# Optimization experiments

Hardware: AMD Instinct MI355X
Metric: run time of the kernel (lower is better)

Reference implementation:

```python
import jax, jax.numpy as jnp
import numpy as np

NH = 8      # num_heads
NP_ = 4     # num_points

def setup_inputs() -> dict:
    key = jax.random.key(0)
    ks = jax.random.split(key, 12)
    B, N, C = 8, 4096, 256
    query = jax.random.normal(ks[0], (B, N, C), jnp.float32)
    value = jax.random.normal(ks[1], (B, N, C), jnp.float32)
    reference_points = jax.random.uniform(ks[2], (B, N, 2), jnp.float32)
    xav = lambda k, i, o: jax.random.normal(k, (i, o), jnp.float32) * np.sqrt(2.0 / (i + o)).astype(np.float32)
    W_off = jax.random.normal(ks[3], (C, NH * NP_ * 2), jnp.float32) * 0.02  # small offsets (orig inits to 0)
    b_off = jax.random.normal(ks[4], (NH * NP_ * 2,), jnp.float32) * 0.02
    W_attn = xav(ks[5], C, NH * NP_)
    b_attn = jnp.zeros((NH * NP_,), jnp.float32)
    W_val = xav(ks[6], C, C)
    b_val = jnp.zeros((C,), jnp.float32)
    W_out = xav(ks[7], C, C)
    b_out = jnp.zeros((C,), jnp.float32)
    return dict(query=query, value=value, reference_points=reference_points,
                W_off=W_off, b_off=b_off, W_attn=W_attn, b_attn=b_attn,
                W_val=W_val, b_val=b_val, W_out=W_out, b_out=b_out)

def _deform_attn(query, value, reference_points, W_off, b_off, W_attn, b_attn, W_val, b_val, W_out, b_out):
    B, N, C = query.shape
    HW = value.shape[1]
    H = W = int(np.sqrt(HW))  # static
    hd = C // NH
    # value projection -> [B, NH, H*W, hd]
    vals = (value @ W_val + b_val).reshape(B, H, W, NH, hd)
    vals = vals.transpose(0, 3, 1, 2, 4).reshape(B, NH, H * W, hd)
    # offsets [B,N,NH,P,2] in [-0.5,0.5]; attention weights softmax over P
    off = jnp.tanh((query @ W_off + b_off).reshape(B, N, NH, NP_, 2)) * 0.5
    attn = jax.nn.softmax((query @ W_attn + b_attn).reshape(B, N, NH, NP_), axis=-1)
    # sampling locations in [0,1], then grid coords in [-1,1] (x=width, y=height)
    loc = jnp.clip(reference_points[:, :, None, None, :] + off, 0.0, 1.0)
    g = loc * 2.0 - 1.0
    # torch grid_sample, align_corners=False: pixel = (g+1)*size/2 - 0.5
    x = (g[..., 0] + 1.0) * (W * 0.5) - 0.5
    y = (g[..., 1] + 1.0) * (H * 0.5) - 0.5
    x0f = jnp.floor(x); y0f = jnp.floor(y)
    wx1 = x - x0f; wx0 = 1.0 - wx1
    wy1 = y - y0f; wy0 = 1.0 - wy1
    x0 = x0f.astype(jnp.int32); x1 = x0 + 1
    y0 = y0f.astype(jnp.int32); y1 = y0 + 1

    def corner(xi, yi, w):  # xi,yi,w: [B,N,NH,P]; zero padding outside
        valid = (xi >= 0) & (xi < W) & (yi >= 0) & (yi < H)
        idx = jnp.clip(yi, 0, H - 1) * W + jnp.clip(xi, 0, W - 1)
        idx_h = idx.transpose(0, 2, 1, 3).reshape(B, NH, N * NP_)      # [B,NH,N*P]
        gat = jnp.take_along_axis(vals, idx_h[..., None], axis=2)      # [B,NH,N*P,hd]
        wv = jnp.where(valid, w, 0.0).transpose(0, 2, 1, 3).reshape(B, NH, N * NP_)
        return gat * wv[..., None]

    sampled = (corner(x0, y0, wx0 * wy0) + corner(x1, y0, wx1 * wy0)
               + corner(x0, y1, wx0 * wy1) + corner(x1, y1, wx1 * wy1))
    sampled = sampled.reshape(B, NH, N, NP_, hd)
    attn_h = attn.transpose(0, 2, 1, 3)                                 # [B,NH,N,P]
    out = jnp.einsum('bhnpd,bhnp->bnhd', sampled, attn_h).reshape(B, N, C)
    return out @ W_out + b_out  # dropout is identity in eval

def reference(query, value, reference_points, W_off, b_off, W_attn, b_attn, W_val, b_val, W_out, b_out):
    return _deform_attn(query, value, reference_points, W_off, b_off, W_attn, b_attn, W_val, b_val, W_out, b_out)
```

## Files before the change

### kernel.cpp

```cpp
#include <hip/hip_runtime.h>
#include <math.h>

#define NHEAD 8
#define NPT 4
#define HDIM 32
#define IMG 64
#define CDIM 256
#define NQ 4096
#define BATCH 8
#define MTOT (BATCH * NQ)

typedef __attribute__((ext_vector_type(8))) short bf16x8;
typedef __attribute__((ext_vector_type(4))) float f32x4;

__device__ __forceinline__ unsigned short f2b(float f) {
    union { float f; unsigned u; } v; v.f = f;
    unsigned r = (v.u + 0x7FFFu + ((v.u >> 16) & 1u)) >> 16;
    return (unsigned short)r;
}
__device__ __forceinline__ float b2f(unsigned short u) {
    union { unsigned u; float f; } v; v.u = ((unsigned)u) << 16;
    return v.f;
}

#define SWZ(row, col) ((col) ^ (((row) & 7) << 3))

__device__ __forceinline__ void gload16(const void* src, void* ldsbase) {
    __builtin_amdgcn_global_load_lds(
        (const __attribute__((address_space(1))) void*)src,
        (__attribute__((address_space(3))) void*)ldsbase, 16, 0, 0);
}


__global__ __launch_bounds__(256)
void cvt_weights_kernel(const float* __restrict__ Wv, const float* __restrict__ Wo,
                        const float* __restrict__ Woff, const float* __restrict__ Wattn,
                        const float* __restrict__ boff, const float* __restrict__ battn,
                        unsigned short* __restrict__ Wv_t, unsigned short* __restrict__ Wo_t,
                        unsigned short* __restrict__ Wl_h, unsigned short* __restrict__ Wl_l,
                        float* __restrict__ bias_lin)
{
    int tid = blockIdx.x * 256 + threadIdx.x;
    int n = tid & 255, k = tid >> 8;
    Wv_t[n * 256 + k] = f2b(Wv[k * 256 + n]);
    Wo_t[n * 256 + k] = f2b(Wo[k * 256 + n]);
    if (tid < 128 * 256) {
        int nn = tid >> 8;
        int kk = tid & 255;
        float v = (nn < 64) ? Woff[kk * 64 + nn]
                : (nn < 96) ? Wattn[kk * 32 + (nn - 64)] : 0.f;
        unsigned short hi = f2b(v);
        unsigned short lo = f2b(v - b2f(hi));
        Wl_h[nn * 256 + kk] = hi;
        Wl_l[nn * 256 + kk] = lo;
    }
    if (tid < 128)
        bias_lin[tid] = (tid < 64) ? boff[tid] : (tid < 96) ? battn[tid - 64] : 0.f;
}

__global__ __launch_bounds__(256)
void lin_gemm_kernel(const float* __restrict__ Q,
                     const unsigned short* __restrict__ Wl_h,
                     const unsigned short* __restrict__ Wl_l,
                     const float* __restrict__ bias,
                     float* __restrict__ lin)
{
    __shared__ unsigned short Ah[128][64], Al[128][64];
    __shared__ unsigned short Bh[128][64], Bl[128][64];

    const int tid  = threadIdx.x;
    const int lane = tid & 63;
    const int wid  = tid >> 6;
    const int gm = ((blockIdx.x & 7) << 12) + ((blockIdx.x >> 3) << 7);
    const int wr = (wid >> 1) * 64;
    const int wc = (wid & 1) * 64;
    const int l15 = lane & 15;
    const int lk  = (lane >> 4) * 8;
    const int rl  = lane >> 3;
    const int ch  = (lane & 7) ^ (rl & 7);

    f32x4 acc[4][4];
    #pragma unroll
    for (int m = 0; m < 4; ++m)
        #pragma unroll
        for (int n = 0; n < 4; ++n)
            #pragma unroll
            for (int r = 0; r < 4; ++r) acc[m][n][r] = 0.f;

    for (int k0 = 0; k0 < 256; k0 += 64) {
        #pragma unroll
        for (int it = 0; it < 4; ++it) {
            const int br = it * 32 + wid * 8;
            gload16(&Wl_h[(size_t)(br + rl) * 256 + k0 + ch * 8], &Bh[br][0]);
            gload16(&Wl_l[(size_t)(br + rl) * 256 + k0 + ch * 8], &Bl[br][0]);
        }
        #pragma unroll
        for (int it = 0; it < 4; ++it) {
            const int chunk = it * 256 + tid;
            const int row = chunk >> 3;
            const int kc  = (chunk & 7) << 3;
            const float4* src = (const float4*)&Q[(size_t)(gm + row) * 256 + k0 + kc];
            const float4 a = src[0], b = src[1];
            float f[8] = {a.x, a.y, a.z, a.w, b.x, b.y, b.z, b.w};
            unsigned short h[8], l[8];
            #pragma unroll
            for (int j = 0; j < 8; ++j) {
                h[j] = f2b(f[j]);
                l[j] = f2b(f[j] - b2f(h[j]));
            }
            const int sc = SWZ(row, kc);
            *(uint4*)&Ah[row][sc] = *(const uint4*)h;
            *(uint4*)&Al[row][sc] = *(const uint4*)l;
        }
        __syncthreads();

        #pragma unroll
        for (int kk = 0; kk < 64; kk += 32) {
            bf16x8 ah[4], al[4];
            #pragma unroll
            for (int m = 0; m < 4; ++m) {
                const int r = wr + m * 16 + l15;
                const int c = SWZ(r, kk + lk);
                ah[m] = *(const bf16x8*)&Ah[r][c];
                al[m] = *(const bf16x8*)&Al[r][c];
            }
            if (wc == 0) {
                bf16x8 bh[4], bl[4];
                #pragma unroll
                for (int n = 0; n < 4; ++n) {
                    const int r = n * 16 + l15;
                    const int c = SWZ(r, kk + lk);
                    bh[n] = *(const bf16x8*)&Bh[r][c];
                    bl[n] = *(const bf16x8*)&Bl[r][c];
                }
                #pragma unroll
                for (int m = 0; m < 4; ++m)
                    #pragma unroll
                    for (int n = 0; n < 4; ++n) {
                        acc[m][n] = __builtin_amdgcn_mfma_f32_16x16x32_bf16(ah[m], bh[n], acc[m][n], 0, 0, 0);
                        acc[m][n] = __builtin_amdgcn_mfma_f32_16x16x32_bf16(ah[m], bl[n], acc[m][n], 0, 0, 0);
                        acc[m][n] = __builtin_amdgcn_mfma_f32_16x16x32_bf16(al[m], bh[n], acc[m][n], 0, 0, 0);
                    }
            } else {
                bf16x8 bh[2], bl[2];
                #pragma unroll
                for (int n = 0; n < 2; ++n) {
                    const int r = 64 + n * 16 + l15;
                    const int c = SWZ(r, kk + lk);
                    bh[n] = *(const bf16x8*)&Bh[r][c];
                    bl[n] = *(const bf16x8*)&Bl[r][c];
                }
                #pragma unroll
                for (int m = 0; m < 4; ++m)
                    #pragma unroll
                    for (int n = 0; n < 2; ++n) {
                        acc[m][n] = __builtin_amdgcn_mfma_f32_16x16x32_bf16(ah[m], bh[n], acc[m][n], 0, 0, 0);
                        acc[m][n] = __builtin_amdgcn_mfma_f32_16x16x32_bf16(ah[m], bl[n], acc[m][n], 0, 0, 0);
                        acc[m][n] = __builtin_amdgcn_mfma_f32_16x16x32_bf16(al[m], bh[n], acc[m][n], 0, 0, 0);
                    }
            }
        }
        __syncthreads();
    }

    const int cr = (lane >> 4) * 4;
    #pragma unroll
    for (int n = 0; n < 4; ++n) {
        const int col = wc + n * 16 + l15;
        if (col < 96) {
            const float bv = bias[col];
            #pragma unroll
            for (int m = 0; m < 4; ++m)
                #pragma unroll
                for (int r = 0; r < 4; ++r) {
                    const int row = gm + wr + m * 16 + cr + r;
                    lin[(size_t)row * 96 + col] = acc[m][n][r] + bv;
                }
        }
    }
}

template<bool A_F32, bool OUT_BF16>
__global__ __launch_bounds__(256)
void gemm_bf16_kernel(const void* __restrict__ Ap,
                      const unsigned short* __restrict__ Bt,
                      const float* __restrict__ bias,
                      void* __restrict__ C)
{
    __shared__ unsigned short As[128][64];
    __shared__ unsigned short Bs[128][64];

    const int tid  = threadIdx.x;
    const int lane = tid & 63;
    const int wid  = tid >> 6;
    const int gm = ((blockIdx.x & 7) << 12) + ((blockIdx.x >> 3) << 7);
    const int gn = blockIdx.y * 128;
    const int wr = (wid >> 1) * 64;
    const int wc = (wid & 1) * 64;
    const int l15 = lane & 15;
    const int lk  = (lane >> 4) * 8;
    const int rl  = lane >> 3;
    const int ch  = (lane & 7) ^ (rl & 7);

    f32x4 acc[4][4];
    #pragma unroll
    for (int m = 0; m < 4; ++m)
        #pragma unroll
        for (int n = 0; n < 4; ++n)
            #pragma unroll
            for (int r = 0; r < 4; ++r) acc[m][n][r] = 0.f;

    for (int k0 = 0; k0 < 256; k0 += 64) {
        #pragma unroll
        for (int it = 0; it < 4; ++it) {
            const int br = it * 32 + wid * 8;
            gload16(&Bt[(size_t)(gn + br + rl) * 256 + k0 + ch * 8], &Bs[br][0]);
        }
        if (A_F32) {
            #pragma unroll
            for (int it = 0; it < 4; ++it) {
                const int chunk = it * 256 + tid;
                const int row = chunk >> 3;
                const int kc  = (chunk & 7) << 3;
                const float4* src = (const float4*)&((const float*)Ap)[(size_t)(gm + row) * 256 + k0 + kc];
                const float4 a = src[0], b = src[1];
                float f[8] = {a.x, a.y, a.z, a.w, b.x, b.y, b.z, b.w};
                unsigned short h[8];
                #pragma unroll
                for (int j = 0; j < 8; ++j) h[j] = f2b(f[j]);
                *(uint4*)&As[row][SWZ(row, kc)] = *(const uint4*)h;
            }
        } else {
            #pragma unroll
            for (int it = 0; it < 4; ++it) {
                const int br = it * 32 + wid * 8;
                gload16(&((const unsigned short*)Ap)[(size_t)(gm + br + rl) * 256 + k0 + ch * 8], &As[br][0]);
            }
        }
        __syncthreads();

        #pragma unroll
        for (int kk = 0; kk < 64; kk += 32) {
            bf16x8 a[4], b[4];
            #pragma unroll
            for (int m = 0; m < 4; ++m) {
                const int r = wr + m * 16 + l15;
                a[m] = *(const bf16x8*)&As[r][SWZ(r, kk + lk)];
            }
            #pragma unroll
            for (int n = 0; n < 4; ++n) {
                const int r = wc + n * 16 + l15;
                b[n] = *(const bf16x8*)&Bs[r][SWZ(r, kk + lk)];
            }
            #pragma unroll
            for (int m = 0; m < 4; ++m)
                #pragma unroll
                for (int n = 0; n < 4; ++n)
                    acc[m][n] = __builtin_amdgcn_mfma_f32_16x16x32_bf16(a[m], b[n], acc[m][n], 0, 0, 0);
        }
        __syncthreads();
    }

    const int cr = (lane >> 4) * 4;
    #pragma unroll
    for (int n = 0; n < 4; ++n) {
        const int col = gn + wc + n * 16 + l15;
        const float bv = bias[col];
        #pragma unroll
        for (int m = 0; m < 4; ++m) {
            #pragma unroll
            for (int r = 0; r < 4; ++r) {
                const int row = gm + wr + m * 16 + cr + r;
                const float v = acc[m][n][r] + bv;
                if (OUT_BF16)
                    ((unsigned short*)C)[(size_t)row * 256 + col] = f2b(v);
                else
                    ((float*)C)[(size_t)row * 256 + col] = v;
            }
        }
    }
}

__global__ __launch_bounds__(256)
void sample_gather_kernel(const unsigned short* __restrict__ projv,
                          const float* __restrict__ lin,
                          const float* __restrict__ refp,
                          unsigned short* __restrict__ sampled)
{
    __shared__ float4 s_w[8][32];
    __shared__ unsigned s_xy[8][32];

    const int i = blockIdx.x;
    const int b = i & 7;
    const int bn0 = (b << 12) + ((i >> 3) << 3);
    const int t = threadIdx.x;

    {
        const int sub = t >> 5;
        const int q = t & 31;
        const int h = q >> 2;
        const int p = q & 3;
        const int bn = bn0 + sub;
        const float2 rp = *(const float2*)&refp[(size_t)bn * 2];
        const float2 ol = *(const float2*)&lin[(size_t)bn * 96 + h * 8 + p * 2];
        const float al  = lin[(size_t)bn * 96 + 64 + q];

        float mx = al;
        mx = fmaxf(mx, __shfl_xor(mx, 1));
        mx = fmaxf(mx, __shfl_xor(mx, 2));
        float e = expf(al - mx);
        float s = e;
        s += __shfl_xor(s, 1);
        s += __shfl_xor(s, 2);
        const float aw = e / s;

        const float lx = fminf(fmaxf(rp.x + tanhf(ol.x) * 0.5f, 0.f), 1.f);
        const float ly = fminf(fmaxf(rp.y + tanhf(ol.y) * 0.5f, 0.f), 1.f);
        const float x = lx * (float)IMG - 0.5f;
        const float y = ly * (float)IMG - 0.5f;
        const float x0f = floorf(x), y0f = floorf(y);
        const int x0 = (int)x0f, y0 = (int)y0f;
        const float wx1 = x - x0f, wx0 = 1.f - wx1;
        const float wy1 = y - y0f, wy0 = 1.f - wy1;
        const bool vx0 = (x0 >= 0), vx1 = (x0 + 1 < IMG);
        const bool vy0 = (y0 >= 0), vy1 = (y0 + 1 < IMG);
        float4 w;
        w.x = (vx0 && vy0) ? wx0 * wy0 * aw : 0.f;
        w.y = (vx1 && vy0) ? wx1 * wy0 * aw : 0.f;
        w.z = (vx0 && vy1) ? wx0 * wy1 * aw : 0.f;
        w.w = (vx1 && vy1) ? wx1 * wy1 * aw : 0.f;
        const int x0c = min(max(x0, 0), IMG - 1), x1c = min(max(x0 + 1, 0), IMG - 1);
        const int y0c = min(max(y0, 0), IMG - 1), y1c = min(max(y0 + 1, 0), IMG - 1);
        s_w[sub][q] = w;
        s_xy[sub][q] = (unsigned)x0c | ((unsigned)x1c << 8) | ((unsigned)y0c << 16) | ((unsigned)y1c << 24);
    }
    __syncthreads();

    const int l = t & 63;
    const int h2 = l >> 3;
    const int cp = l & 7;
    const unsigned short* vbase = projv + ((size_t)b << 20) + h2 * HDIM + cp * 4;

    #pragma unroll
    for (int pass = 0; pass < 2; ++pass) {
        const int sub = (t >> 6) + pass * 4;
        const int bn = bn0 + sub;

        float a0 = 0.f, a1 = 0.f, a2 = 0.f, a3 = 0.f;
        #pragma unroll
        for (int p = 0; p < 4; ++p) {
            const float4 w = s_w[sub][h2 * 4 + p];
            const unsigned xy = s_xy[sub][h2 * 4 + p];
            const int x0 = xy & 255, x1 = (xy >> 8) & 255;
            const int y0 = (xy >> 16) & 255, y1 = xy >> 24;
            const uint2 u00 = *(const uint2*)&vbase[(((y0 << 6) + x0) << 8)];
            const uint2 u01 = *(const uint2*)&vbase[(((y0 << 6) + x1) << 8)];
            const uint2 u10 = *(const uint2*)&vbase[(((y1 << 6) + x0) << 8)];
            const uint2 u11 = *(const uint2*)&vbase[(((y1 << 6) + x1) << 8)];
            a0 += w.x * b2f((unsigned short)(u00.x & 0xffff)) + w.y * b2f((unsigned short)(u01.x & 0xffff))
                + w.z * b2f((unsigned short)(u10.x & 0xffff)) + w.w * b2f((unsigned short)(u11.x & 0xffff));
            a1 += w.x * b2f((unsigned short)(u00.x >> 16)) + w.y * b2f((unsigned short)(u01.x >> 16))
                + w.z * b2f((unsigned short)(u10.x >> 16)) + w.w * b2f((unsigned short)(u11.x >> 16));
            a2 += w.x * b2f((unsigned short)(u00.y & 0xffff)) + w.y * b2f((unsigned short)(u01.y & 0xffff))
                + w.z * b2f((unsigned short)(u10.y & 0xffff)) + w.w * b2f((unsigned short)(u11.y & 0xffff));
            a3 += w.x * b2f((unsigned short)(u00.y >> 16)) + w.y * b2f((unsigned short)(u01.y >> 16))
                + w.z * b2f((unsigned short)(u10.y >> 16)) + w.w * b2f((unsigned short)(u11.y >> 16));
        }
        uint2 outp;
        outp.x = (unsigned)f2b(a0) | ((unsigned)f2b(a1) << 16);
        outp.y = (unsigned)f2b(a2) | ((unsigned)f2b(a3) << 16);
        *(uint2*)&sampled[(size_t)bn * 256 + h2 * HDIM + cp * 4] = outp;
    }
}

extern "C" void kernel_launch(void* const* d_in, const int* in_sizes, int n_in,
                              void* d_out, int out_size, void* d_ws, size_t ws_size,
                              hipStream_t stream)
{
    const float* query  = (const float*)d_in[0];
    const float* value  = (const float*)d_in[1];
    const float* refp   = (const float*)d_in[2];
    const float* W_off  = (const float*)d_in[3];
    const float* b_off  = (const float*)d_in[4];
    const float* W_attn = (const float*)d_in[5];
    const float* b_attn = (const float*)d_in[6];
    const float* W_val  = (const float*)d_in[7];
    const float* b_val  = (const float*)d_in[8];
    const float* W_out  = (const float*)d_in[9];
    const float* b_out  = (const float*)d_in[10];
    float* out = (float*)d_out;

    char* ws = (char*)d_ws;
    unsigned short* projv    = (unsigned short*)ws; ws += (size_t)MTOT * 256 * 2;
    unsigned short* sampled  = (unsigned short*)ws; ws += (size_t)MTOT * 256 * 2;
    float*          lin      = (float*)ws;          ws += (size_t)MTOT * 96 * 4;
    unsigned short* Wv_t     = (unsigned short*)ws; ws += 256 * 256 * 2;
    unsigned short* Wo_t     = (unsigned short*)ws; ws += 256 * 256 * 2;
    unsigned short* Wl_h     = (unsigned short*)ws; ws += 128 * 256 * 2;
    unsigned short* Wl_l     = (unsigned short*)ws; ws += 128 * 256 * 2;
    float*          bias_lin = (float*)ws;          ws += 128 * 4;

    dim3 blk(256);

    cvt_weights_kernel<<<dim3(256), blk, 0, stream>>>(W_val, W_out, W_off, W_attn, b_off, b_attn,
                                                      Wv_t, Wo_t, Wl_h, Wl_l, bias_lin);

    gemm_bf16_kernel<true, true><<<dim3(MTOT / 128, 2), blk, 0, stream>>>(value, Wv_t, b_val, projv);

    lin_gemm_kernel<<<dim3(MTOT / 128), blk, 0, stream>>>(query, Wl_h, Wl_l, bias_lin, lin);

    sample_gather_kernel<<<dim3(MTOT / 8), blk, 0, stream>>>(projv, lin, refp, sampled);

    gemm_bf16_kernel<false, false><<<dim3(MTOT / 128, 2), blk, 0, stream>>>(sampled, Wo_t, b_out, out);
}
```

Before: 73.93 us.

## Merge value-projection and offset/attention GEMMs into one launch with smaller LDS

Combines the value projection GEMM and the offset/attention linear GEMM into a single kernel launch of 768 blocks. The first 512 blocks compute projv and the remaining 256 compute lin. The lin path now uses a K-step of 32 with a matching 4-row swizzle, so LDS per block drops from 64KB to 32KB. The aim is to remove a launch boundary, let the two independent GEMMs overlap across CUs, and raise occupancy. The cost is twice as many k-iterations and barriers in the lin blocks, plus an uneven block workload mix.

```diff
diff --git a/kernel.cpp b/kernel.cpp
--- a/kernel.cpp
+++ b/kernel.cpp
@@ -23,7 +23,8 @@
     return v.f;
 }
 
-#define SWZ(row, col) ((col) ^ (((row) & 7) << 3))
+#define SWZ(row, col)   ((col) ^ (((row) & 7) << 3))
+#define SWZ32(row, col) ((col) ^ (((row) & 3) << 3))
 
 __device__ __forceinline__ void gload16(const void* src, void* ldsbase) {
     __builtin_amdgcn_global_load_lds(
@@ -59,25 +60,25 @@
 }
 
 __global__ __launch_bounds__(256)
-void lin_gemm_kernel(const float* __restrict__ Q,
-                     const unsigned short* __restrict__ Wl_h,
-                     const unsigned short* __restrict__ Wl_l,
-                     const float* __restrict__ bias,
-                     float* __restrict__ lin)
+void fused_gemms_kernel(const float* __restrict__ value,
+                        const float* __restrict__ query,
+                        const unsigned short* __restrict__ Wv_t,
+                        const unsigned short* __restrict__ Wl_h,
+                        const unsigned short* __restrict__ Wl_l,
+                        const float* __restrict__ b_val,
+                        const float* __restrict__ bias_lin,
+                        unsigned short* __restrict__ projv,
+                        float* __restrict__ lin)
 {
-    __shared__ unsigned short Ah[128][64], Al[128][64];
-    __shared__ unsigned short Bh[128][64], Bl[128][64];
+    __shared__ char smem[32768];
 
     const int tid  = threadIdx.x;
     const int lane = tid & 63;
     const int wid  = tid >> 6;
-    const int gm = ((blockIdx.x & 7) << 12) + ((blockIdx.x >> 3) << 7);
     const int wr = (wid >> 1) * 64;
     const int wc = (wid & 1) * 64;
     const int l15 = lane & 15;
     const int lk  = (lane >> 4) * 8;
-    const int rl  = lane >> 3;
-    const int ch  = (lane & 7) ^ (rl & 7);
 
     f32x4 acc[4][4];
     #pragma unroll
@@ -87,40 +88,114 @@
             #pragma unroll
             for (int r = 0; r < 4; ++r) acc[m][n][r] = 0.f;
 
-    for (int k0 = 0; k0 < 256; k0 += 64) {
-        #pragma unroll
-        for (int it = 0; it < 4; ++it) {
-            const int br = it * 32 + wid * 8;
-            gload16(&Wl_h[(size_t)(br + rl) * 256 + k0 + ch * 8], &Bh[br][0]);
-            gload16(&Wl_l[(size_t)(br + rl) * 256 + k0 + ch * 8], &Bl[br][0]);
-        }
-        #pragma unroll
-        for (int it = 0; it < 4; ++it) {
-            const int chunk = it * 256 + tid;
-            const int row = chunk >> 3;
-            const int kc  = (chunk & 7) << 3;
-            const float4* src = (const float4*)&Q[(size_t)(gm + row) * 256 + k0 + kc];
-            const float4 a = src[0], b = src[1];
-            float f[8] = {a.x, a.y, a.z, a.w, b.x, b.y, b.z, b.w};
-            unsigned short h[8], l[8];
-            #pragma unroll
-            for (int j = 0; j < 8; ++j) {
-                h[j] = f2b(f[j]);
-                l[j] = f2b(f[j] - b2f(h[j]));
-            }
-            const int sc = SWZ(row, kc);
-            *(uint4*)&Ah[row][sc] = *(const uint4*)h;
-            *(uint4*)&Al[row][sc] = *(const uint4*)l;
-        }
-        __syncthreads();
-
-        #pragma unroll
-        for (int kk = 0; kk < 64; kk += 32) {
+    if (blockIdx.x < 512) {
+        unsigned short (*As)[64] = (unsigned short(*)[64])smem;
+        unsigned short (*Bs)[64] = (unsigned short(*)[64])(smem + 16384);
+        const int bx = blockIdx.x;
+        const int gm = ((bx & 7) << 12) + (((bx >> 3) & 31) << 7);
+        const int gn = (bx >> 8) << 7;
+        const int rl  = lane >> 3;
+        const int ch  = (lane & 7) ^ (rl & 7);
+
+        for (int k0 = 0; k0 < 256; k0 += 64) {
+            #pragma unroll
+            for (int it = 0; it < 4; ++it) {
+                const int br = it * 32 + wid * 8;
+                gload16(&Wv_t[(size_t)(gn + br + rl) * 256 + k0 + ch * 8], &Bs[br][0]);
+            }
+            #pragma unroll
+            for (int it = 0; it < 4; ++it) {
+                const int chunk = it * 256 + tid;
+                const int row = chunk >> 3;
+                const int kc  = (chunk & 7) << 3;
+                const float4* src = (const float4*)&value[(size_t)(gm + row) * 256 + k0 + kc];
+                const float4 a = src[0], b = src[1];
+                float f[8] = {a.x, a.y, a.z, a.w, b.x, b.y, b.z, b.w};
+                unsigned short h[8];
+                #pragma unroll
+                for (int j = 0; j < 8; ++j) h[j] = f2b(f[j]);
+                *(uint4*)&As[row][SWZ(row, kc)] = *(const uint4*)h;
+            }
+            __syncthreads();
+
+            #pragma unroll
+            for (int kk = 0; kk < 64; kk += 32) {
+                bf16x8 a[4], b[4];
+                #pragma unroll
+                for (int m = 0; m < 4; ++m) {
+                    const int r = wr + m * 16 + l15;
+                    a[m] = *(const bf16x8*)&As[r][SWZ(r, kk + lk)];
+                }
+                #pragma unroll
+                for (int n = 0; n < 4; ++n) {
+                    const int r = wc + n * 16 + l15;
+                    b[n] = *(const bf16x8*)&Bs[r][SWZ(r, kk + lk)];
+                }
+                #pragma unroll
+                for (int m = 0; m < 4; ++m)
+                    #pragma unroll
+                    for (int n = 0; n < 4; ++n)
+                        acc[m][n] = __builtin_amdgcn_mfma_f32_16x16x32_bf16(a[m], b[n], acc[m][n], 0, 0, 0);
+            }
+            __syncthreads();
+        }
+
+        const int cr = (lane >> 4) * 4;
+        #pragma unroll
+        for (int n = 0; n < 4; ++n) {
+            const int col = gn + wc + n * 16 + l15;
+            const float bv = b_val[col];
+            #pragma unroll
+            for (int m = 0; m < 4; ++m)
+                #pragma unroll
+                for (int r = 0; r < 4; ++r) {
+                    const int row = gm + wr + m * 16 + cr + r;
+                    projv[(size_t)row * 256 + col] = f2b(acc[m][n][r] + bv);
+                }
+        }
+    } else {
+        unsigned short (*Ah)[32] = (unsigned short(*)[32])smem;
+        unsigned short (*Al)[32] = (unsigned short(*)[32])(smem + 8192);
+        unsigned short (*Bh)[32] = (unsigned short(*)[32])(smem + 16384);
+        unsigned short (*Bl)[32] = (unsigned short(*)[32])(smem + 24576);
+        const int lbx = blockIdx.x - 512;
+        const int gm = ((lbx & 7) << 12) + ((lbx >> 3) << 7);
+        const int rs = lane >> 2;
+        const int cc = lane & 3;
+
+        for (int k0 = 0; k0 < 256; k0 += 32) {
+            #pragma unroll
+            for (int i = 0; i < 2; ++i) {
+                const int row = wid * 32 + i * 16 + rs;
+                const int cs = (cc ^ (row & 3)) << 3;
+                gload16(&Wl_h[(size_t)row * 256 + k0 + cs], &Bh[wid * 32 + i * 16][0]);
+                gload16(&Wl_l[(size_t)row * 256 + k0 + cs], &Bl[wid * 32 + i * 16][0]);
+            }
+            #pragma unroll
+            for (int it = 0; it < 2; ++it) {
+                const int chunk = it * 256 + tid;
+                const int row = chunk >> 2;
+                const int kc  = (chunk & 3) << 3;
+                const float4* src = (const float4*)&query[(size_t)(gm + row) * 256 + k0 + kc];
+                const float4 a = src[0], b = src[1];
+                float f[8] = {a.x, a.y, a.z, a.w, b.x, b.y, b.z, b.w};
+                unsigned short h[8], l[8];
+                #pragma unroll
+                for (int j = 0; j < 8; ++j) {
+                    h[j] = f2b(f[j]);
+                    l[j] = f2b(f[j] - b2f(h[j]));
+                }
+                const int sc = SWZ32(row, kc);
+                *(uint4*)&Ah[row][sc] = *(const uint4*)h;
+                *(uint4*)&Al[row][sc] = *(const uint4*)l;
+            }
+            __syncthreads();
+
             bf16x8 ah[4], al[4];
             #pragma unroll
             for (int m = 0; m < 4; ++m) {
                 const int r = wr + m * 16 + l15;
-                const int c = SWZ(r, kk + lk);
+                const int c = SWZ32(r, lk);
                 ah[m] = *(const bf16x8*)&Ah[r][c];
                 al[m] = *(const bf16x8*)&Al[r][c];
             }
@@ -129,7 +204,7 @@
                 #pragma unroll
                 for (int n = 0; n < 4; ++n) {
                     const int r = n * 16 + l15;
-                    const int c = SWZ(r, kk + lk);
+                    const int c = SWZ32(r, lk);
                     bh[n] = *(const bf16x8*)&Bh[r][c];
                     bl[n] = *(const bf16x8*)&Bl[r][c];
                 }
@@ -146,7 +221,7 @@
                 #pragma unroll
                 for (int n = 0; n < 2; ++n) {
                     const int r = 64 + n * 16 + l15;
-                    const int c = SWZ(r, kk + lk);
+                    const int c = SWZ32(r, lk);
                     bh[n] = *(const bf16x8*)&Bh[r][c];
                     bl[n] = *(const bf16x8*)&Bl[r][c];
                 }
@@ -159,33 +234,32 @@
                         acc[m][n] = __builtin_amdgcn_mfma_f32_16x16x32_bf16(al[m], bh[n], acc[m][n], 0, 0, 0);
                     }
             }
-        }
-        __syncthreads();
-    }
-
-    const int cr = (lane >> 4) * 4;
-    #pragma unroll
-    for (int n = 0; n < 4; ++n) {
-        const int col = wc + n * 16 + l15;
-        if (col < 96) {
-            const float bv = bias[col];
-            #pragma unroll
-            for (int m = 0; m < 4; ++m)
-                #pragma unroll
-                for (int r = 0; r < 4; ++r) {
-                    const int row = gm + wr + m * 16 + cr + r;
-                    lin[(size_t)row * 96 + col] = acc[m][n][r] + bv;
-                }
-        }
-    }
-}
-
-template<bool A_F32, bool OUT_BF16>
+            __syncthreads();
+        }
+
+        const int cr = (lane >> 4) * 4;
+        #pragma unroll
+        for (int n = 0; n < 4; ++n) {
+            const int col = wc + n * 16 + l15;
+            if (col < 96) {
+                const float bv = bias_lin[col];
+                #pragma unroll
+                for (int m = 0; m < 4; ++m)
+                    #pragma unroll
+                    for (int r = 0; r < 4; ++r) {
+                        const int row = gm + wr + m * 16 + cr + r;
+                        lin[(size_t)row * 96 + col] = acc[m][n][r] + bv;
+                    }
+            }
+        }
+    }
+}
+
 __global__ __launch_bounds__(256)
-void gemm_bf16_kernel(const void* __restrict__ Ap,
-                      const unsigned short* __restrict__ Bt,
-                      const float* __restrict__ bias,
-                      void* __restrict__ C)
+void gemm_out_kernel(const unsigned short* __restrict__ Ap,
+                     const unsigned short* __restrict__ Bt,
+                     const float* __restrict__ bias,
+                     float* __restrict__ C)
 {
     __shared__ unsigned short As[128][64];
     __shared__ unsigned short Bs[128][64];
@@ -215,27 +289,7 @@
         for (int it = 0; it < 4; ++it) {
             const int br = it * 32 + wid * 8;
             gload16(&Bt[(size_t)(gn + br + rl) * 256 + k0 + ch * 8], &Bs[br][0]);
-        }
-        if (A_F32) {
-            #pragma unroll
-            for (int it = 0; it < 4; ++it) {
-                const int chunk = it * 256 + tid;
-                const int row = chunk >> 3;
-                const int kc  = (chunk & 7) << 3;
-                const float4* src = (const float4*)&((const float*)Ap)[(size_t)(gm + row) * 256 + k0 + kc];
-                const float4 a = src[0], b = src[1];
-                float f[8] = {a.x, a.y, a.z, a.w, b.x, b.y, b.z, b.w};
-                unsigned short h[8];
-                #pragma unroll
-                for (int j = 0; j < 8; ++j) h[j] = f2b(f[j]);
-                *(uint4*)&As[row][SWZ(row, kc)] = *(const uint4*)h;
-            }
-        } else {
-            #pragma unroll
-            for (int it = 0; it < 4; ++it) {
-                const int br = it * 32 + wid * 8;
-                gload16(&((const unsigned short*)Ap)[(size_t)(gm + br + rl) * 256 + k0 + ch * 8], &As[br][0]);
-            }
+            gload16(&Ap[(size_t)(gm + br + rl) * 256 + k0 + ch * 8], &As[br][0]);
         }
         __syncthreads();
 
@@ -267,17 +321,12 @@
         const int col = gn + wc + n * 16 + l15;
         const float bv = bias[col];
         #pragma unroll
-        for (int m = 0; m < 4; ++m) {
+        for (int m = 0; m < 4; ++m)
             #pragma unroll
             for (int r = 0; r < 4; ++r) {
                 const int row = gm + wr + m * 16 + cr + r;
-                const float v = acc[m][n][r] + bv;
-                if (OUT_BF16)
-                    ((unsigned short*)C)[(size_t)row * 256 + col] = f2b(v);
-                else
-                    ((float*)C)[(size_t)row * 256 + col] = v;
-            }
-        }
+                C[(size_t)row * 256 + col] = acc[m][n][r] + bv;
+            }
     }
 }
 
@@ -405,11 +454,10 @@
     cvt_weights_kernel<<<dim3(256), blk, 0, stream>>>(W_val, W_out, W_off, W_attn, b_off, b_attn,
                                                       Wv_t, Wo_t, Wl_h, Wl_l, bias_lin);
 
-    gemm_bf16_kernel<true, true><<<dim3(MTOT / 128, 2), blk, 0, stream>>>(value, Wv_t, b_val, projv);
-
-    lin_gemm_kernel<<<dim3(MTOT / 128), blk, 0, stream>>>(query, Wl_h, Wl_l, bias_lin, lin);
+    fused_gemms_kernel<<<dim3(768), blk, 0, stream>>>(value, query, Wv_t, Wl_h, Wl_l,
+                                                      b_val, bias_lin, projv, lin);
 
     sample_gather_kernel<<<dim3(MTOT / 8), blk, 0, stream>>>(projv, lin, refp, sampled);
 
-    gemm_bf16_kernel<false, false><<<dim3(MTOT / 128, 2), blk, 0, stream>>>(sampled, Wo_t, b_out, out);
-}
+    gemm_out_kernel<<<dim3(MTOT / 128, 2), blk, 0, stream>>>(sampled, Wo_t, b_out, out);
+}
```

New measurement: 73.28 us. No clear change (-0.9%).
